# Optimization experiments

Hardware: AMD Instinct MI355X
Metric: run time of the kernel (lower is better)

The kernel has to match this reference:

```python
import jax, jax.numpy as jnp
import numpy as np

H, D, K = 8, 64, 9           # new num heads, head size, conv kernel size
A = H * D                    # all_head_size = 512
HID = 2 * A                  # input hidden size = 1024
STD = 0.02


def setup_inputs() -> dict:
    key = jax.random.key(0)
    ks = jax.random.split(key, 16)
    B, S = 4, 2048
    f = jnp.float32
    inp = {
        'hidden_states': jax.random.normal(ks[0], (B, S, HID), f),
        'Wq': jax.random.normal(ks[1], (A, A), f) * STD,
        'bq': jnp.zeros((A,), f),
        'Wk': jax.random.normal(ks[2], (A, A), f) * STD,
        'bk': jnp.zeros((A,), f),
        'Wv': jax.random.normal(ks[3], (A, A), f) * STD,
        'bv': jnp.zeros((A,), f),
        'dw_w': jax.random.normal(ks[4], (A, 1, K), f) * STD,   # depthwise conv (groups=A)
        'pw_w': jax.random.normal(ks[5], (A, A, 1), f) * STD,   # pointwise 1x1 conv
        'sep_b': jnp.zeros((A, 1), f),                          # SeparableConv1D bias
        'Wck': jax.random.normal(ks[6], (H * K, A), f) * STD,   # conv_kernel_layer
        'bck': jnp.zeros((H * K,), f),
        'Wco': jax.random.normal(ks[7], (A, A), f) * STD,       # conv_out_layer
        'bco': jnp.zeros((A,), f),
    }
    return inp


def reference(hidden_states, Wq, bq, Wk, bk, Wv, bv, dw_w, pw_w, sep_b, Wck, bck, Wco, bco):
    B, S, _ = hidden_states.shape
    hs_attn = hidden_states[:, :, :A]
    hs_conv = hidden_states[:, :, A:]

    q = hs_attn @ Wq.T + bq
    k = hs_attn @ Wk.T + bk
    v = hs_attn @ Wv.T + bv

    # SeparableConv1D on (B, A, S): depthwise then pointwise, plus bias
    x = hs_conv.transpose(0, 2, 1)
    x = jax.lax.conv_general_dilated(
        x, dw_w, window_strides=(1,), padding=[(K // 2, K // 2)],
        feature_group_count=A, dimension_numbers=('NCH', 'OIH', 'NCH'))
    x = jnp.einsum('bcs,oc->bos', x, pw_w[:, :, 0]) + sep_b
    mixed_key_conv = x.transpose(0, 2, 1)            # (B,S,A)

    # per-token softmax conv kernel
    conv_attn = mixed_key_conv * hs_conv
    ckl = (conv_attn @ Wck.T + bck).reshape(B, S, H, K)
    ckl = jax.nn.softmax(ckl, axis=-1)               # softmax over kernel taps

    # dynamic-span lightweight convolution (unfold -> batched matmul)
    col = hs_conv @ Wco.T + bco                      # (B,S,A)
    pad = jnp.pad(col, ((0, 0), (K // 2, K // 2), (0, 0)))
    windows = jnp.stack([pad[:, i:i + S] for i in range(K)], axis=-1)  # (B,S,A,K)
    windows = windows.reshape(B, S, H, D, K)
    conv_out = jnp.einsum('bshdk,bshk->bshd', windows, ckl)            # (B,S,H,D)

    # standard self-attention
    qh = q.reshape(B, S, H, D).transpose(0, 2, 1, 3)
    kh = k.reshape(B, S, H, D).transpose(0, 2, 1, 3)
    vh = v.reshape(B, S, H, D).transpose(0, 2, 1, 3)
    scale = jnp.asarray(1.0 / np.sqrt(D), q.dtype)
    scores = jnp.einsum('bhqd,bhkd->bhqk', qh, kh) * scale
    probs = jax.nn.softmax(scores, axis=-1)
    ctx = jnp.einsum('bhqk,bhkd->bqhd', probs, vh)   # (B,S,H,D)

    out = jnp.concatenate([ctx, conv_out], axis=2)   # (B,S,2H,D)
    return out.reshape(B, S, HID)
```

## Files before the change

kernel.cpp:

```cpp
#include <hip/hip_runtime.h>
#include <hip/hip_bf16.h>

#define NH   8
#define HD   64
#define KW   9
#define AD   512
#define HIDD 1024
#define BB   4
#define SS   2048
#define MTOK (BB*SS)
#define WSZ  262144

typedef __attribute__((ext_vector_type(8))) short short8;
typedef __attribute__((ext_vector_type(4))) float floatx4;

__device__ __forceinline__ short f2bf(float f) {
    unsigned u = __float_as_uint(f);
    u = (u + 0x7FFFu + ((u >> 16) & 1u)) >> 16;
    return (short)u;
}
__device__ __forceinline__ float bf2f(short s) {
    return __uint_as_float(((unsigned)(unsigned short)s) << 16);
}
__device__ __forceinline__ float exp2_raw(float x) {
    return __builtin_amdgcn_exp2f(x);
}
__device__ __forceinline__ unsigned pkbf2(float a, float b) {
    unsigned au = __float_as_uint(a) + 0x8000u;
    unsigned bu = __float_as_uint(b) + 0x8000u;
    return __builtin_amdgcn_perm(bu, au, 0x07060302);
}
__device__ __forceinline__ void gl2lds16(const short* g, short* l) {
    __builtin_amdgcn_global_load_lds(
        (const __attribute__((address_space(1))) void*)g,
        (__attribute__((address_space(3))) void*)l, 16, 0, 0);
}

__global__ __launch_bounds__(256) void cvt_hs_kernel(
    const float* __restrict__ hs, short* __restrict__ hsb)
{
    int idx = blockIdx.x * 256 + threadIdx.x;
    const float* s = hs + (long)idx * 8;
    float4 a = *(const float4*)s, c = *(const float4*)(s + 4);
    short8 o;
    o[0]=f2bf(a.x); o[1]=f2bf(a.y); o[2]=f2bf(a.z); o[3]=f2bf(a.w);
    o[4]=f2bf(c.x); o[5]=f2bf(c.y); o[6]=f2bf(c.z); o[7]=f2bf(c.w);
    *(short8*)(hsb + (long)idx * 8) = o;
}

__global__ __launch_bounds__(256) void cvt_w_kernel(
    const float* __restrict__ pw, const float* __restrict__ Wco,
    const float* __restrict__ Wq, const float* __restrict__ Wk,
    const float* __restrict__ Wv, const float* __restrict__ Wck,
    const float* __restrict__ dw,
    short* __restrict__ dst, float* __restrict__ dwT)
{
    int idx = blockIdx.x * 256 + threadIdx.x;
    if (idx >= 172032) {
        int t = idx - 172032;
        if (t < AD * KW) {
            int c = t / KW, k = t - c * KW;
            dwT[k * AD + c] = dw[t];
        }
        return;
    }
    int e0 = idx * 8;
    short8 o;
    if (e0 < 5 * WSZ) {
        int w = e0 >> 18, off = e0 & (WSZ - 1);
        const float* src = (w == 0) ? pw : (w == 1) ? Wco : (w == 2) ? Wq
                         : (w == 3) ? Wk : Wv;
        float4 a = *(const float4*)(src + off), c = *(const float4*)(src + off + 4);
        o[0]=f2bf(a.x); o[1]=f2bf(a.y); o[2]=f2bf(a.z); o[3]=f2bf(a.w);
        o[4]=f2bf(c.x); o[5]=f2bf(c.y); o[6]=f2bf(c.z); o[7]=f2bf(c.w);
    } else {
        int off = e0 - 5 * WSZ;
        int row = off >> 9, col = off & 511;
        if (row < NH * KW) {
            const float* src = Wck + row * AD + col;
            float4 a = *(const float4*)src, c = *(const float4*)(src + 4);
            o[0]=f2bf(a.x); o[1]=f2bf(a.y); o[2]=f2bf(a.z); o[3]=f2bf(a.w);
            o[4]=f2bf(c.x); o[5]=f2bf(c.y); o[6]=f2bf(c.z); o[7]=f2bf(c.w);
        } else {
            for (int i = 0; i < 8; ++i) o[i] = 0;
        }
    }
    *(short8*)(dst + e0) = o;
}

__global__ __launch_bounds__(256) void dwconv_kernel(
    const short* __restrict__ hsb, const float* __restrict__ dwT,
    short* __restrict__ x1)
{
    int idx = blockIdx.x * 256 + threadIdx.x;
    int c8  = (idx & 63) * 8;
    int tok = idx >> 6;
    int s   = tok & (SS - 1);
    int b   = tok >> 11;
    const short* base = hsb + (long)(b * SS) * HIDD + AD + c8;
    float acc[8];
#pragma unroll
    for (int i = 0; i < 8; ++i) acc[i] = 0.f;
#pragma unroll
    for (int kk = 0; kk < KW; ++kk) {
        int ss2 = s + kk - KW / 2;
        if (ss2 >= 0 && ss2 < SS) {
            short8 hv = *(const short8*)(base + (long)ss2 * HIDD);
            float4 w0 = *(const float4*)(dwT + kk * AD + c8);
            float4 w1 = *(const float4*)(dwT + kk * AD + c8 + 4);
            acc[0] += w0.x * bf2f(hv[0]); acc[1] += w0.y * bf2f(hv[1]);
            acc[2] += w0.z * bf2f(hv[2]); acc[3] += w0.w * bf2f(hv[3]);
            acc[4] += w1.x * bf2f(hv[4]); acc[5] += w1.y * bf2f(hv[5]);
            acc[6] += w1.z * bf2f(hv[6]); acc[7] += w1.w * bf2f(hv[7]);
        }
    }
    short8 o;
#pragma unroll
    for (int i = 0; i < 8; ++i) o[i] = f2bf(acc[i]);
    *(short8*)(x1 + (long)tok * AD + c8) = o;
}

template<int FM, int FN, int MODE>
__global__ __launch_bounds__(256) void gemm_bf16_kernel(
    const short* __restrict__ X, int ldx, int xoff,
    const short* __restrict__ W,
    const float* __restrict__ b0p, const float* __restrict__ b1p,
    const float* __restrict__ b2p,
    const short* __restrict__ mulp, int mul_ld, int mul_off,
    void* __restrict__ Cout, short* __restrict__ vtout,
    int ldc, int N, int Kd, float oscale)
{
    constexpr int TM = 32 * FM, TN = 32 * FN;
    __shared__ __align__(16) short As[TM * 64];
    __shared__ __align__(16) short Bs[TN * 64];
    const int tid  = threadIdx.x;
    const int wv   = tid >> 6, lane = tid & 63;
    const int ln   = lane & 15, quad = lane >> 4;
    const int wm   = wv >> 1, wn = wv & 1;
    const int m0 = blockIdx.x * TM, n0 = blockIdx.y * TN;

    floatx4 acc[FM][FN];
#pragma unroll
    for (int i = 0; i < FM; ++i)
#pragma unroll
        for (int j = 0; j < FN; ++j) acc[i][j] = (floatx4){0.f, 0.f, 0.f, 0.f};

    const short* xbase = X + (long)m0 * ldx + xoff;
    const short* wbase = W + (long)n0 * Kd;

    for (int k0 = 0; k0 < Kd; k0 += 64) {
#pragma unroll
        for (int g = tid; g < TM * 8; g += 256) {
            int m = g >> 3, p = g & 7, gk = p ^ (m & 7);
            gl2lds16(xbase + (long)m * ldx + k0 + gk * 8, &As[g * 8]);
        }
#pragma unroll
        for (int g = tid; g < TN * 8; g += 256) {
            int m = g >> 3, p = g & 7, gk = p ^ (m & 7);
            gl2lds16(wbase + (long)m * Kd + k0 + gk * 8, &Bs[g * 8]);
        }
        __syncthreads();
#pragma unroll
        for (int half = 0; half < 2; ++half) {
            short8 afr[FM], bfr[FN];
#pragma unroll
            for (int i = 0; i < FM; ++i) {
                int p = (half * 4 + quad) ^ (ln & 7);
                afr[i] = *(const short8*)&As[(wm * 16 * FM + i * 16 + ln) * 64 + p * 8];
            }
#pragma unroll
            for (int j = 0; j < FN; ++j) {
                int p = (half * 4 + quad) ^ (ln & 7);
                bfr[j] = *(const short8*)&Bs[(wn * 16 * FN + j * 16 + ln) * 64 + p * 8];
            }
#pragma unroll
            for (int i = 0; i < FM; ++i)
#pragma unroll
                for (int j = 0; j < FN; ++j)
                    acc[i][j] = __builtin_amdgcn_mfma_f32_16x16x32_bf16(
                        afr[i], bfr[j], acc[i][j], 0, 0, 0);
        }
        __syncthreads();
    }

#pragma unroll
    for (int j = 0; j < FN; ++j) {
        int n = n0 + wn * 16 * FN + j * 16 + ln;
        if constexpr (MODE == 3) {
            if (n >= 1024) {
                int hh = (n - 1024) >> 6, dd = (n - 1024) & 63;
                float bv = b2p[n - 1024];
                int mblk = m0 + wm * 16 * FM;
                int bidx = mblk >> 11, sblk = mblk & (SS - 1);
                short* dst = vtout + ((long)((bidx * NH + hh) * HD + dd)) * SS + sblk;
#pragma unroll
                for (int r = 0; r < 4; ++r) {
                    unsigned lo = pkbf2(acc[0][j][r] + bv, acc[1 % FM][j][r] + bv);
                    unsigned hi = pkbf2(acc[2 % FM][j][r] + bv, acc[3 % FM][j][r] + bv);
                    *(uint2*)(dst + (quad * 4 + r) * 4) = make_uint2(lo, hi);
                }
            } else {
                float bv = (n < 512) ? b0p[n] : b1p[n - 512];
                float sc = (n < 512) ? oscale : 1.f;
#pragma unroll
                for (int i = 0; i < FM; ++i) {
#pragma unroll
                    for (int r = 0; r < 4; ++r) {
                        int m = m0 + wm * 16 * FM + i * 16 + quad * 4 + r;
                        float val = (acc[i][j][r] + bv) * sc;
                        ((short*)Cout)[(long)m * ldc + n] = f2bf(val);
                    }
                }
            }
        } else if (n < N) {
            float bv = b0p[n], sc = oscale;
#pragma unroll
            for (int i = 0; i < FM; ++i) {
#pragma unroll
                for (int r = 0; r < 4; ++r) {
                    int m = m0 + wm * 16 * FM + i * 16 + quad * 4 + r;
                    float val = (acc[i][j][r] + bv) * sc;
                    if constexpr (MODE == 2)
                        val *= bf2f(mulp[(long)m * mul_ld + mul_off + n]);
                    if constexpr (MODE == 0)
                        ((float*)Cout)[(long)m * ldc + n] = val;
                    else
                        ((short*)Cout)[(long)m * ldc + n] = f2bf(val);
                }
            }
        }
    }
}

__global__ __launch_bounds__(256) void convout_kernel(
    const short* __restrict__ col, const float* __restrict__ ckl,
    float* __restrict__ out)
{
    int idx = blockIdx.x * 256 + threadIdx.x;
    int d4  = (idx & 127) * 4;
    int tok = idx >> 7;
    int s   = tok & (SS - 1);
    int b   = tok >> 11;
    int h   = d4 >> 6;
    const float* lg = ckl + (long)tok * (NH * KW) + h * KW;
    float wv[KW];
    float mx = -1e30f;
#pragma unroll
    for (int i = 0; i < KW; ++i) { wv[i] = lg[i]; mx = fmaxf(mx, wv[i]); }
    float sum = 0.f;
#pragma unroll
    for (int i = 0; i < KW; ++i) { wv[i] = __expf(wv[i] - mx); sum += wv[i]; }
    float inv = 1.f / sum;
    float a0 = 0.f, a1 = 0.f, a2 = 0.f, a3 = 0.f;
    const short* cbase = col + (long)(b * SS) * AD + d4;
#pragma unroll
    for (int kk = 0; kk < KW; ++kk) {
        int ss2 = s + kk - KW / 2;
        if (ss2 >= 0 && ss2 < SS) {
            uint2 cv = *(const uint2*)(cbase + (long)ss2 * AD);
            float w = wv[kk];
            a0 += w * bf2f((short)(cv.x & 0xFFFF));
            a1 += w * bf2f((short)(cv.x >> 16));
            a2 += w * bf2f((short)(cv.y & 0xFFFF));
            a3 += w * bf2f((short)(cv.y >> 16));
        }
    }
    *(float4*)&out[(long)tok * HIDD + AD + d4] =
        make_float4(a0 * inv, a1 * inv, a2 * inv, a3 * inv);
}

__global__ __launch_bounds__(256) void flash_mfma_kernel(
    const short* __restrict__ qkv, const short* __restrict__ vT,
    float* __restrict__ out)
{
    const int qt = blockIdx.x, h = blockIdx.y, b = blockIdx.z;
    const int tid  = threadIdx.x;
    const int w    = tid >> 6;
    const int lane = tid & 63;
    const int ln   = lane & 15;
    const int quad = lane >> 4;

    __shared__ __align__(16) short Kb[64 * 64];
    __shared__ __align__(16) short Vt[64 * 64];
    __shared__ __align__(16) short Ps[4][16 * 72];

    const int  q0 = qt * 64;
    const long rowbase = (long)b * SS;

    short8 qa[2];
    {
        const short* qrow = qkv + (rowbase + q0 + w * 16 + ln) * 1536 + h * HD;
        qa[0] = *(const short8*)(qrow + quad * 8);
        qa[1] = *(const short8*)(qrow + 32 + quad * 8);
    }

    floatx4 acc[4];
    float l_i[4];
#pragma unroll
    for (int r = 0; r < 4; ++r) {
        l_i[r] = 0.f;
        acc[r] = (floatx4){0.f, 0.f, 0.f, 0.f};
    }

    const short* kbase  = qkv + 512 + rowbase * 1536 + h * HD;
    const short* vtbase = vT + ((long)(b * NH + h) * HD) * SS;

    for (int kt = 0; kt < SS / 64; ++kt) {
        const int k0 = kt * 64;
#pragma unroll
        for (int it = 0; it < 2; ++it) {
            int g = it * 256 + tid;
            int m = g >> 3, p = g & 7, gk = p ^ (m & 7);
            gl2lds16(kbase + (long)(k0 + m) * 1536 + gk * 8, &Kb[g * 8]);
        }
#pragma unroll
        for (int it = 0; it < 2; ++it) {
            int g = it * 256 + tid;
            int m = g >> 3, p = g & 7, gk = p ^ (m & 7);
            gl2lds16(vtbase + (long)m * SS + k0 + gk * 8, &Vt[g * 8]);
        }
        __syncthreads();

        floatx4 S[4];
#pragma unroll
        for (int st = 0; st < 4; ++st) {
            int p0i = quad ^ (ln & 7), p1i = (4 + quad) ^ (ln & 7);
            short8 b0 = *(const short8*)&Kb[(st * 16 + ln) * 64 + p0i * 8];
            short8 b1 = *(const short8*)&Kb[(st * 16 + ln) * 64 + p1i * 8];
            floatx4 z = (floatx4){0.f, 0.f, 0.f, 0.f};
            z = __builtin_amdgcn_mfma_f32_16x16x32_bf16(qa[0], b0, z, 0, 0, 0);
            S[st] = __builtin_amdgcn_mfma_f32_16x16x32_bf16(qa[1], b1, z, 0, 0, 0);
        }

#pragma unroll
        for (int r = 0; r < 4; ++r) {
            float p0 = exp2_raw(S[0][r]);
            float p1 = exp2_raw(S[1][r]);
            float p2 = exp2_raw(S[2][r]);
            float p3 = exp2_raw(S[3][r]);
            l_i[r] += (p0 + p1) + (p2 + p3);
            unsigned lo = pkbf2(p0, p1);
            unsigned hi = pkbf2(p2, p3);
            *(uint2*)&Ps[w][(quad * 4 + r) * 72 + ln * 4] = make_uint2(lo, hi);
        }

        {
            short8 pa0 = *(const short8*)&Ps[w][ln * 72 + quad * 8];
            short8 pa1 = *(const short8*)&Ps[w][ln * 72 + 32 + quad * 8];
#pragma unroll
            for (int st = 0; st < 4; ++st) {
                int p0i = quad ^ (ln & 7), p1i = (4 + quad) ^ (ln & 7);
                short8 vb0 = *(const short8*)&Vt[(st * 16 + ln) * 64 + p0i * 8];
                short8 vb1 = *(const short8*)&Vt[(st * 16 + ln) * 64 + p1i * 8];
                acc[st] = __builtin_amdgcn_mfma_f32_16x16x32_bf16(pa0, vb0, acc[st], 0, 0, 0);
                acc[st] = __builtin_amdgcn_mfma_f32_16x16x32_bf16(pa1, vb1, acc[st], 0, 0, 0);
            }
        }
        __syncthreads();
    }

#pragma unroll
    for (int r = 0; r < 4; ++r) {
#pragma unroll
        for (int off = 1; off < 16; off <<= 1)
            l_i[r] += __shfl_xor(l_i[r], off);
    }

#pragma unroll
    for (int r = 0; r < 4; ++r) {
        float inv = 1.f / l_i[r];
        float* orow = out + (rowbase + q0 + w * 16 + quad * 4 + r) * HIDD + h * HD;
#pragma unroll
        for (int st = 0; st < 4; ++st)
            orow[st * 16 + ln] = acc[st][r] * inv;
    }
}

extern "C" void kernel_launch(void* const* d_in, const int* in_sizes, int n_in,
                              void* d_out, int out_size, void* d_ws, size_t ws_size,
                              hipStream_t stream)
{
    const float* hs   = (const float*)d_in[0];
    const float* Wq   = (const float*)d_in[1];
    const float* bq   = (const float*)d_in[2];
    const float* Wk   = (const float*)d_in[3];
    const float* bk   = (const float*)d_in[4];
    const float* Wv   = (const float*)d_in[5];
    const float* bv   = (const float*)d_in[6];
    const float* dw   = (const float*)d_in[7];
    const float* pw   = (const float*)d_in[8];
    const float* sepb = (const float*)d_in[9];
    const float* Wck  = (const float*)d_in[10];
    const float* bck  = (const float*)d_in[11];
    const float* Wco  = (const float*)d_in[12];
    const float* bco  = (const float*)d_in[13];
    float* out = (float*)d_out;

    short* hsb  = (short*)d_ws;
    short* x1c  = hsb + (long)MTOK * HIDD;
    short* qkvb = x1c + (long)MTOK * AD;
    short* vTb  = qkvb + (long)MTOK * 1536;
    float* ckl  = (float*)(vTb + (long)MTOK * AD);
    short* wb   = (short*)(ckl + (long)MTOK * (NH * KW));
    short* pw_b   = wb;
    short* Wco_b  = wb + 1L * WSZ;
    short* Wqkv_b = wb + 2L * WSZ;
    short* Wck_b  = wb + 5L * WSZ;
    float* dwT    = (float*)(Wck_b + 128L * AD);
    short* cab    = qkvb;

    const float QSCALE = 0.18033688011112042f;

    cvt_hs_kernel<<<MTOK * HIDD / 2048, 256, 0, stream>>>(hs, hsb);
    cvt_w_kernel<<<690, 256, 0, stream>>>(
        pw, Wco, Wq, Wk, Wv, Wck, dw, wb, dwT);
    dwconv_kernel<<<MTOK * AD / 2048, 256, 0, stream>>>(hsb, dwT, x1c);
    gemm_bf16_kernel<2, 2, 2><<<dim3(MTOK / 64, AD / 64), 256, 0, stream>>>(
        x1c, AD, 0, pw_b, sepb, nullptr, nullptr, hsb, HIDD, AD,
        cab, nullptr, AD, AD, AD, 1.f);
    gemm_bf16_kernel<2, 2, 0><<<dim3(MTOK / 64, 2), 256, 0, stream>>>(
        cab, AD, 0, Wck_b, bck, nullptr, nullptr, nullptr, 0, 0,
        ckl, nullptr, NH * KW, NH * KW, AD, 1.f);
    gemm_bf16_kernel<2, 2, 1><<<dim3(MTOK / 64, AD / 64), 256, 0, stream>>>(
        hsb, HIDD, AD, Wco_b, bco, nullptr, nullptr, nullptr, 0, 0,
        x1c, nullptr, AD, AD, AD, 1.f);
    convout_kernel<<<MTOK * AD / 1024, 256, 0, stream>>>(x1c, ckl, out);
    gemm_bf16_kernel<4, 4, 3><<<dim3(MTOK / 128, 1536 / 128), 256, 0, stream>>>(
        hsb, HIDD, 0, Wqkv_b, bq, bk, bv, nullptr, 0, 0,
        qkvb, vTb, 1536, 1536, AD, QSCALE);
    flash_mfma_kernel<<<dim3(SS / 64, NH, BB), 256, 0, stream>>>(qkvb, vTb, out);

    (void)in_sizes; (void)n_in; (void)out_size; (void)ws_size;
}
```

Before: 230.9 us.

## Fuse hidden-state conversion with depthwise conv and double flash query tile

Merges the fp32-to-bf16 conversion of hidden states with the depthwise convolution into one kernel that reads fp32 directly, removing a launch and a bf16 round-trip read. The depthwise conv now accumulates from fp32 inputs instead of rounded bf16. The flash attention kernel now gives each wave 32 query rows instead of 16, so each block covers 128 queries and every K/V tile loaded into LDS serves twice as many MFMAs. The cost is higher register pressure and half as many blocks (512) for the attention grid.

```diff
diff --git a/kernel.cpp b/kernel.cpp
--- a/kernel.cpp
+++ b/kernel.cpp
@@ -34,18 +34,6 @@
     __builtin_amdgcn_global_load_lds(
         (const __attribute__((address_space(1))) void*)g,
         (__attribute__((address_space(3))) void*)l, 16, 0, 0);
-}
-
-__global__ __launch_bounds__(256) void cvt_hs_kernel(
-    const float* __restrict__ hs, short* __restrict__ hsb)
-{
-    int idx = blockIdx.x * 256 + threadIdx.x;
-    const float* s = hs + (long)idx * 8;
-    float4 a = *(const float4*)s, c = *(const float4*)(s + 4);
-    short8 o;
-    o[0]=f2bf(a.x); o[1]=f2bf(a.y); o[2]=f2bf(a.z); o[3]=f2bf(a.w);
-    o[4]=f2bf(c.x); o[5]=f2bf(c.y); o[6]=f2bf(c.z); o[7]=f2bf(c.w);
-    *(short8*)(hsb + (long)idx * 8) = o;
 }
 
 __global__ __launch_bounds__(256) void cvt_w_kernel(
@@ -88,36 +76,50 @@
     *(short8*)(dst + e0) = o;
 }
 
-__global__ __launch_bounds__(256) void dwconv_kernel(
-    const short* __restrict__ hsb, const float* __restrict__ dwT,
-    short* __restrict__ x1)
+__global__ __launch_bounds__(256) void cvt_dw_kernel(
+    const float* __restrict__ hs, const float* __restrict__ dwT,
+    short* __restrict__ hsb, short* __restrict__ x1)
 {
     int idx = blockIdx.x * 256 + threadIdx.x;
-    int c8  = (idx & 63) * 8;
-    int tok = idx >> 6;
-    int s   = tok & (SS - 1);
-    int b   = tok >> 11;
-    const short* base = hsb + (long)(b * SS) * HIDD + AD + c8;
-    float acc[8];
-#pragma unroll
-    for (int i = 0; i < 8; ++i) acc[i] = 0.f;
-#pragma unroll
-    for (int kk = 0; kk < KW; ++kk) {
-        int ss2 = s + kk - KW / 2;
-        if (ss2 >= 0 && ss2 < SS) {
-            short8 hv = *(const short8*)(base + (long)ss2 * HIDD);
-            float4 w0 = *(const float4*)(dwT + kk * AD + c8);
-            float4 w1 = *(const float4*)(dwT + kk * AD + c8 + 4);
-            acc[0] += w0.x * bf2f(hv[0]); acc[1] += w0.y * bf2f(hv[1]);
-            acc[2] += w0.z * bf2f(hv[2]); acc[3] += w0.w * bf2f(hv[3]);
-            acc[4] += w1.x * bf2f(hv[4]); acc[5] += w1.y * bf2f(hv[5]);
-            acc[6] += w1.z * bf2f(hv[6]); acc[7] += w1.w * bf2f(hv[7]);
-        }
-    }
+    int c8  = (idx & 127) * 8;
+    int tok = idx >> 7;
+    const float* s = hs + (long)tok * HIDD + c8;
+    float4 a = *(const float4*)s, c = *(const float4*)(s + 4);
     short8 o;
-#pragma unroll
-    for (int i = 0; i < 8; ++i) o[i] = f2bf(acc[i]);
-    *(short8*)(x1 + (long)tok * AD + c8) = o;
+    o[0]=f2bf(a.x); o[1]=f2bf(a.y); o[2]=f2bf(a.z); o[3]=f2bf(a.w);
+    o[4]=f2bf(c.x); o[5]=f2bf(c.y); o[6]=f2bf(c.z); o[7]=f2bf(c.w);
+    *(short8*)(hsb + (long)tok * HIDD + c8) = o;
+
+    if (c8 >= AD) {
+        int cc = c8 - AD;
+        int ss = tok & (SS - 1), b = tok >> 11;
+        float acc[8];
+        {
+            const float* w0 = dwT + 4 * AD + cc;
+            acc[0] = w0[0]*a.x; acc[1] = w0[1]*a.y;
+            acc[2] = w0[2]*a.z; acc[3] = w0[3]*a.w;
+            acc[4] = w0[4]*c.x; acc[5] = w0[5]*c.y;
+            acc[6] = w0[6]*c.z; acc[7] = w0[7]*c.w;
+        }
+#pragma unroll
+        for (int kk = 0; kk < KW; ++kk) {
+            if (kk == 4) continue;
+            int ss2 = ss + kk - KW / 2;
+            if (ss2 >= 0 && ss2 < SS) {
+                const float* src = hs + ((long)(b * SS + ss2)) * HIDD + c8;
+                float4 h0 = *(const float4*)src, h1 = *(const float4*)(src + 4);
+                const float* w0 = dwT + kk * AD + cc;
+                acc[0] += w0[0]*h0.x; acc[1] += w0[1]*h0.y;
+                acc[2] += w0[2]*h0.z; acc[3] += w0[3]*h0.w;
+                acc[4] += w0[4]*h1.x; acc[5] += w0[5]*h1.y;
+                acc[6] += w0[6]*h1.z; acc[7] += w0[7]*h1.w;
+            }
+        }
+        short8 ov;
+#pragma unroll
+        for (int i = 0; i < 8; ++i) ov[i] = f2bf(acc[i]);
+        *(short8*)(x1 + (long)tok * AD + cc) = ov;
+    }
 }
 
 template<int FM, int FN, int MODE>
@@ -282,28 +284,32 @@
 
     __shared__ __align__(16) short Kb[64 * 64];
     __shared__ __align__(16) short Vt[64 * 64];
-    __shared__ __align__(16) short Ps[4][16 * 72];
-
-    const int  q0 = qt * 64;
+    __shared__ __align__(16) short Ps[4][32 * 72];
+
+    const int  q0 = qt * 128;
     const long rowbase = (long)b * SS;
 
-    short8 qa[2];
-    {
-        const short* qrow = qkv + (rowbase + q0 + w * 16 + ln) * 1536 + h * HD;
-        qa[0] = *(const short8*)(qrow + quad * 8);
-        qa[1] = *(const short8*)(qrow + 32 + quad * 8);
-    }
-
-    floatx4 acc[4];
-    float l_i[4];
-#pragma unroll
-    for (int r = 0; r < 4; ++r) {
-        l_i[r] = 0.f;
-        acc[r] = (floatx4){0.f, 0.f, 0.f, 0.f};
-    }
+    short8 qa[2][2];
+#pragma unroll
+    for (int u = 0; u < 2; ++u) {
+        const short* qrow = qkv + (rowbase + q0 + w * 32 + u * 16 + ln) * 1536 + h * HD;
+        qa[u][0] = *(const short8*)(qrow + quad * 8);
+        qa[u][1] = *(const short8*)(qrow + 32 + quad * 8);
+    }
+
+    floatx4 acc[2][4];
+    float l_i[2][4];
+#pragma unroll
+    for (int u = 0; u < 2; ++u)
+#pragma unroll
+        for (int r = 0; r < 4; ++r) {
+            l_i[u][r] = 0.f;
+            acc[u][r] = (floatx4){0.f, 0.f, 0.f, 0.f};
+        }
 
     const short* kbase  = qkv + 512 + rowbase * 1536 + h * HD;
     const short* vtbase = vT + ((long)(b * NH + h) * HD) * SS;
+    const int p0i = quad ^ (ln & 7), p1i = (4 + quad) ^ (ln & 7);
 
     for (int kt = 0; kt < SS / 64; ++kt) {
         const int k0 = kt * 64;
@@ -321,59 +327,68 @@
         }
         __syncthreads();
 
-        floatx4 S[4];
+        floatx4 S[2][4];
 #pragma unroll
         for (int st = 0; st < 4; ++st) {
-            int p0i = quad ^ (ln & 7), p1i = (4 + quad) ^ (ln & 7);
             short8 b0 = *(const short8*)&Kb[(st * 16 + ln) * 64 + p0i * 8];
             short8 b1 = *(const short8*)&Kb[(st * 16 + ln) * 64 + p1i * 8];
-            floatx4 z = (floatx4){0.f, 0.f, 0.f, 0.f};
-            z = __builtin_amdgcn_mfma_f32_16x16x32_bf16(qa[0], b0, z, 0, 0, 0);
-            S[st] = __builtin_amdgcn_mfma_f32_16x16x32_bf16(qa[1], b1, z, 0, 0, 0);
-        }
-
-#pragma unroll
-        for (int r = 0; r < 4; ++r) {
-            float p0 = exp2_raw(S[0][r]);
-            float p1 = exp2_raw(S[1][r]);
-            float p2 = exp2_raw(S[2][r]);
-            float p3 = exp2_raw(S[3][r]);
-            l_i[r] += (p0 + p1) + (p2 + p3);
-            unsigned lo = pkbf2(p0, p1);
-            unsigned hi = pkbf2(p2, p3);
-            *(uint2*)&Ps[w][(quad * 4 + r) * 72 + ln * 4] = make_uint2(lo, hi);
-        }
+#pragma unroll
+            for (int u = 0; u < 2; ++u) {
+                floatx4 z = (floatx4){0.f, 0.f, 0.f, 0.f};
+                z = __builtin_amdgcn_mfma_f32_16x16x32_bf16(qa[u][0], b0, z, 0, 0, 0);
+                S[u][st] = __builtin_amdgcn_mfma_f32_16x16x32_bf16(qa[u][1], b1, z, 0, 0, 0);
+            }
+        }
+
+#pragma unroll
+        for (int u = 0; u < 2; ++u)
+#pragma unroll
+            for (int r = 0; r < 4; ++r) {
+                float p0 = exp2_raw(S[u][0][r]);
+                float p1 = exp2_raw(S[u][1][r]);
+                float p2 = exp2_raw(S[u][2][r]);
+                float p3 = exp2_raw(S[u][3][r]);
+                l_i[u][r] += (p0 + p1) + (p2 + p3);
+                unsigned lo = pkbf2(p0, p1);
+                unsigned hi = pkbf2(p2, p3);
+                *(uint2*)&Ps[w][(u * 16 + quad * 4 + r) * 72 + ln * 4] =
+                    make_uint2(lo, hi);
+            }
 
         {
-            short8 pa0 = *(const short8*)&Ps[w][ln * 72 + quad * 8];
-            short8 pa1 = *(const short8*)&Ps[w][ln * 72 + 32 + quad * 8];
+            short8 pa[2][2];
+#pragma unroll
+            for (int u = 0; u < 2; ++u) {
+                pa[u][0] = *(const short8*)&Ps[w][(u * 16 + ln) * 72 + quad * 8];
+                pa[u][1] = *(const short8*)&Ps[w][(u * 16 + ln) * 72 + 32 + quad * 8];
+            }
 #pragma unroll
             for (int st = 0; st < 4; ++st) {
-                int p0i = quad ^ (ln & 7), p1i = (4 + quad) ^ (ln & 7);
                 short8 vb0 = *(const short8*)&Vt[(st * 16 + ln) * 64 + p0i * 8];
                 short8 vb1 = *(const short8*)&Vt[(st * 16 + ln) * 64 + p1i * 8];
-                acc[st] = __builtin_amdgcn_mfma_f32_16x16x32_bf16(pa0, vb0, acc[st], 0, 0, 0);
-                acc[st] = __builtin_amdgcn_mfma_f32_16x16x32_bf16(pa1, vb1, acc[st], 0, 0, 0);
+#pragma unroll
+                for (int u = 0; u < 2; ++u) {
+                    acc[u][st] = __builtin_amdgcn_mfma_f32_16x16x32_bf16(pa[u][0], vb0, acc[u][st], 0, 0, 0);
+                    acc[u][st] = __builtin_amdgcn_mfma_f32_16x16x32_bf16(pa[u][1], vb1, acc[u][st], 0, 0, 0);
+                }
             }
         }
         __syncthreads();
     }
 
 #pragma unroll
-    for (int r = 0; r < 4; ++r) {
-#pragma unroll
-        for (int off = 1; off < 16; off <<= 1)
-            l_i[r] += __shfl_xor(l_i[r], off);
-    }
-
-#pragma unroll
-    for (int r = 0; r < 4; ++r) {
-        float inv = 1.f / l_i[r];
-        float* orow = out + (rowbase + q0 + w * 16 + quad * 4 + r) * HIDD + h * HD;
-#pragma unroll
-        for (int st = 0; st < 4; ++st)
-            orow[st * 16 + ln] = acc[st][r] * inv;
-    }
+    for (int u = 0; u < 2; ++u)
+#pragma unroll
+        for (int r = 0; r < 4; ++r) {
+#pragma unroll
+            for (int off = 1; off < 16; off <<= 1)
+                l_i[u][r] += __shfl_xor(l_i[u][r], off);
+            float inv = 1.f / l_i[u][r];
+            float* orow = out + (rowbase + q0 + w * 32 + u * 16 + quad * 4 + r) * HIDD + h * HD;
+#pragma unroll
+            for (int st = 0; st < 4; ++st)
+                orow[st * 16 + ln] = acc[u][st][r] * inv;
+        }
 }
 
 extern "C" void kernel_launch(void* const* d_in, const int* in_sizes, int n_in,
@@ -411,10 +426,9 @@
 
     const float QSCALE = 0.18033688011112042f;
 
-    cvt_hs_kernel<<<MTOK * HIDD / 2048, 256, 0, stream>>>(hs, hsb);
     cvt_w_kernel<<<690, 256, 0, stream>>>(
         pw, Wco, Wq, Wk, Wv, Wck, dw, wb, dwT);
-    dwconv_kernel<<<MTOK * AD / 2048, 256, 0, stream>>>(hsb, dwT, x1c);
+    cvt_dw_kernel<<<MTOK * HIDD / 2048, 256, 0, stream>>>(hs, dwT, hsb, x1c);
     gemm_bf16_kernel<2, 2, 2><<<dim3(MTOK / 64, AD / 64), 256, 0, stream>>>(
         x1c, AD, 0, pw_b, sepb, nullptr, nullptr, hsb, HIDD, AD,
         cab, nullptr, AD, AD, AD, 1.f);
@@ -428,7 +442,7 @@
     gemm_bf16_kernel<4, 4, 3><<<dim3(MTOK / 128, 1536 / 128), 256, 0, stream>>>(
         hsb, HIDD, 0, Wqkv_b, bq, bk, bv, nullptr, 0, 0,
         qkvb, vTb, 1536, 1536, AD, QSCALE);
-    flash_mfma_kernel<<<dim3(SS / 64, NH, BB), 256, 0, stream>>>(qkvb, vTb, out);
+    flash_mfma_kernel<<<dim3(SS / 128, NH, BB), 256, 0, stream>>>(qkvb, vTb, out);
 
     (void)in_sizes; (void)n_in; (void)out_size; (void)ws_size;
 }
```

Measured after the change: 240.6 us. 1.04x slower.
